# Optimization experiments

Hardware: AMD Instinct MI355X
Metric: run time of the kernel (lower is better)

The kernel has to match this reference:

```python
import jax, jax.numpy as jnp
import numpy as np

HIDDEN = 1024
K_STRIDE = 4


def setup_inputs() -> dict:
    key = jax.random.key(0)
    ks = jax.random.split(key, 12)
    N = 8192
    inp = {
        "speech_embed": jax.random.normal(ks[0], (N, HIDDEN * K_STRIDE), dtype=jnp.float32),
        "text_embed": jax.random.normal(ks[1], (N, HIDDEN), dtype=jnp.float32),
        # conv1d(1,1,kernel_size=1,bias=False) weight -> a single scalar
        "conv_w": jax.random.normal(ks[2], (), dtype=jnp.float32),
        # torch Linear weights stored as [in, out] for x @ W + b
        "Wq": jax.random.normal(ks[3], (HIDDEN, HIDDEN), dtype=jnp.float32) * (HIDDEN ** -0.5),
        "bq": jax.random.normal(ks[4], (HIDDEN,), dtype=jnp.float32) * 0.02,
        "Wk": jax.random.normal(ks[5], (HIDDEN, HIDDEN), dtype=jnp.float32) * (HIDDEN ** -0.5),
        "bk": jax.random.normal(ks[6], (HIDDEN,), dtype=jnp.float32) * 0.02,
        "Wv": jax.random.normal(ks[7], (HIDDEN, HIDDEN), dtype=jnp.float32) * (HIDDEN ** -0.5),
        "bv": jax.random.normal(ks[8], (HIDDEN,), dtype=jnp.float32) * 0.02,
        "Wo": jax.random.normal(ks[9], (HIDDEN, HIDDEN), dtype=jnp.float32) * (HIDDEN ** -0.5),
        "bo": jax.random.normal(ks[10], (HIDDEN,), dtype=jnp.float32) * 0.02,
    }
    return inp


def _attention(q, k, v, Wq, bq, Wk, bk, Wv, bv, Wo, bo):
    # Faithful to original: NO 1/sqrt(d) scaling, mask is None.
    q = q @ Wq + bq          # [N, H]
    k = k @ Wk + bk          # [N, H]
    v = v @ Wv + bv          # [N, H]
    weights = jax.nn.softmax(q @ k.T, axis=-1)  # [N, N]
    out = (weights @ v) @ Wo + bo               # [N, H]
    return out, weights


def reference(speech_embed, text_embed, conv_w, Wq, bq, Wk, bk, Wv, bv, Wo, bo):
    # conv1d kernel_size=1, stride=K, no bias == strided subsample * scalar weight
    speech = speech_embed[:, ::K_STRIDE] * conv_w  # [N, HIDDEN]
    tts_out, tts_w = _attention(text_embed, speech, speech,
                                Wq, bq, Wk, bk, Wv, bv, Wo, bo)
    stt_out, stt_w = _attention(speech, text_embed, text_embed,
                                Wq, bq, Wk, bk, Wv, bv, Wo, bo)
    return (tts_out, tts_w, stt_out, stt_w)
```

## Files before the change

### kernel.cpp

```cpp
#include <hip/hip_runtime.h>

#define HID 1024
#define NROW 8192
#define NCAT 16384

typedef unsigned short u16;
typedef short s16x8 __attribute__((ext_vector_type(8)));
typedef float f32x4 __attribute__((ext_vector_type(4)));

__device__ __forceinline__ u16 rtn16(float x) {
  unsigned xb = __builtin_bit_cast(unsigned, x);
  return (u16)((xb + 0x7fffu + ((xb >> 16) & 1u)) >> 16);
}
__device__ __forceinline__ float fromh(u16 h) {
  return __builtin_bit_cast(float, (unsigned)h << 16);
}
__device__ __forceinline__ void split2(float x, u16 &h, u16 &l) {
  h = rtn16(x);
  l = rtn16(x - fromh(h));
}

__device__ __forceinline__ void gl16(const void* g, void* l) {
  __builtin_amdgcn_global_load_lds(
      (const __attribute__((address_space(1))) unsigned int*)g,
      (__attribute__((address_space(3))) unsigned int*)l, 16, 0, 0);
}

template<int N> __device__ __forceinline__ void waitvm() {
  if constexpr (N == 3) asm volatile("s_waitcnt vmcnt(3)" ::: "memory");
  else if constexpr (N == 4) asm volatile("s_waitcnt vmcnt(4)" ::: "memory");
  else if constexpr (N == 5) asm volatile("s_waitcnt vmcnt(5)" ::: "memory");
  else if constexpr (N == 6) asm volatile("s_waitcnt vmcnt(6)" ::: "memory");
}

template<int ROWS>
__device__ __forceinline__ void stage_chunk(const u16* __restrict__ pg, int ld,
                                            int grow0, int k0, u16* ldsbase, int tid)
{
  constexpr int NLD = (ROWS * 32) / (512 * 8);
  #pragma unroll
  for (int j = 0; j < NLD; ++j) {
    int idx = tid + j * 512;
    int row = idx >> 2, q = idx & 3;
    int qs = q ^ ((row >> 1) & 3);
    gl16(pg + (size_t)(grow0 + row) * ld + k0 + qs * 8, ldsbase + (size_t)idx * 8);
  }
}

template<int NFR>
__device__ __forceinline__ void read_frags(s16x8* f, const u16* base,
                                           int w0, int fr, int fq)
{
  #pragma unroll
  for (int i = 0; i < NFR; ++i) {
    int r = w0 + i * 16 + fr;
    f[i] = *(const s16x8*)(base + r * 32 + ((fq ^ ((r >> 1) & 3)) << 3));
  }
}

template<int BN, int WMv, int WNv, int MF, int NF, bool OUT_SPLIT>
__global__ void __launch_bounds__(512, 2)
gemm_big(const u16* __restrict__ Agh, const u16* __restrict__ Agl, int lda,
         const u16* __restrict__ Bgh, const u16* __restrict__ Bgl, int ldb,
         float* __restrict__ Cf, u16* __restrict__ Ch, u16* __restrict__ Cl,
         int ldc, int K, int tiles_n)
{
  constexpr int BM = 256;
  constexpr int ASZ = BM * 32;
  constexpr int BSZ = BN * 32;
  constexpr int BUF = 2 * ASZ + 2 * BSZ;
  constexpr int AL_ = (ASZ * 2) / (512 * 16);
  constexpr int BL_ = (BSZ * 2) / (512 * 16);
  constexpr int TL  = 2 * AL_ + 2 * BL_;
  constexpr int W1 = TL - (AL_ + BL_);
  constexpr int W2 = TL - BL_;
  constexpr int W3 = AL_ + 2 * BL_;

  __shared__ __align__(16) u16 lds[2 * BUF];

  const int tid = threadIdx.x;
  const unsigned nwg = gridDim.x;
  const unsigned bid = blockIdx.x;
  const unsigned swz = (bid & 7u) * (nwg >> 3) + (bid >> 3);
  const int bm = (int)(swz / (unsigned)tiles_n) * BM;
  const int bn = (int)(swz % (unsigned)tiles_n) * BN;

  const int w = tid >> 6, lane = tid & 63;
  const int wr = (w / WNv) * (BM / WMv);
  const int wc = (w % WNv) * (BN / WNv);
  const int fr = lane & 15, fq = lane >> 4;

  f32x4 acc[MF][NF] = {};
  const int nt = K / 32;

  stage_chunk<BM>(Agh, lda, bm, 0, lds + 0,             tid);
  stage_chunk<BN>(Bgh, ldb, bn, 0, lds + 2 * ASZ,       tid);
  stage_chunk<BN>(Bgl, ldb, bn, 0, lds + 2 * ASZ + BSZ, tid);
  stage_chunk<BM>(Agl, lda, bm, 0, lds + ASZ,           tid);

  int cur = 0;
  for (int t = 0; t < nt; ++t) {
    const int k0n = (t + 1 == nt) ? 0 : (t + 1) * 32;
    const int nxt = cur ^ 1;
    u16* cb = lds + cur * BUF;
    u16* nb = lds + nxt * BUF;
    s16x8 ah[MF], bh[NF];

    waitvm<W1>();
    __builtin_amdgcn_s_barrier();
    __builtin_amdgcn_sched_barrier(0);
    stage_chunk<BM>(Agh, lda, bm, k0n, nb + 0,       tid);
    stage_chunk<BN>(Bgh, ldb, bn, k0n, nb + 2 * ASZ, tid);
    read_frags<MF>(ah, cb + 0,       wr, fr, fq);
    read_frags<NF>(bh, cb + 2 * ASZ, wc, fr, fq);
    __builtin_amdgcn_s_setprio(1);
    #pragma unroll
    for (int m = 0; m < MF; ++m)
      #pragma unroll
      for (int n = 0; n < NF; ++n)
        acc[m][n] = __builtin_amdgcn_mfma_f32_16x16x32_bf16(ah[m], bh[n], acc[m][n], 0, 0, 0);
    __builtin_amdgcn_s_setprio(0);

    waitvm<W2>();
    __builtin_amdgcn_s_barrier();
    __builtin_amdgcn_sched_barrier(0);
    stage_chunk<BN>(Bgl, ldb, bn, k0n, nb + 2 * ASZ + BSZ, tid);
    {
      s16x8 bl[NF];
      read_frags<NF>(bl, cb + 2 * ASZ + BSZ, wc, fr, fq);
      __builtin_amdgcn_s_setprio(1);
      #pragma unroll
      for (int m = 0; m < MF; ++m)
        #pragma unroll
        for (int n = 0; n < NF; ++n)
          acc[m][n] = __builtin_amdgcn_mfma_f32_16x16x32_bf16(ah[m], bl[n], acc[m][n], 0, 0, 0);
      __builtin_amdgcn_s_setprio(0);
    }

    waitvm<W3>();
    __builtin_amdgcn_s_barrier();
    __builtin_amdgcn_sched_barrier(0);
    stage_chunk<BM>(Agl, lda, bm, k0n, nb + ASZ, tid);
    {
      s16x8 al[MF];
      read_frags<MF>(al, cb + ASZ, wr, fr, fq);
      __builtin_amdgcn_s_setprio(1);
      #pragma unroll
      for (int m = 0; m < MF; ++m)
        #pragma unroll
        for (int n = 0; n < NF; ++n)
          acc[m][n] = __builtin_amdgcn_mfma_f32_16x16x32_bf16(al[m], bh[n], acc[m][n], 0, 0, 0);
      __builtin_amdgcn_s_setprio(0);
    }
    cur = nxt;
  }

  #pragma unroll
  for (int m = 0; m < MF; ++m) {
    int row0 = bm + wr + m * 16 + fq * 4;
    #pragma unroll
    for (int n = 0; n < NF; ++n) {
      int col = bn + wc + n * 16 + fr;
      if constexpr (OUT_SPLIT) {
        #pragma unroll
        for (int i = 0; i < 4; ++i) {
          u16 h, l; split2(acc[m][n][i], h, l);
          Ch[(size_t)(row0 + i) * ldc + col] = h;
          Cl[(size_t)(row0 + i) * ldc + col] = l;
        }
      } else {
        #pragma unroll
        for (int i = 0; i < 4; ++i)
          Cf[(size_t)(row0 + i) * ldc + col] = acc[m][n][i];
      }
    }
  }
}

template<int AMODE, bool ADD_BIAS, bool WRITE_T, bool OUT_SPLIT>
__global__ void __launch_bounds__(256, 2)
gemm_bt(const u16* __restrict__ Agh, const u16* __restrict__ Agl,
        const float* __restrict__ Agf, int lda,
        const u16* __restrict__ Bgh, const u16* __restrict__ Bgl, int ldb,
        const float* __restrict__ bias,
        float* __restrict__ Cf, u16* __restrict__ Ch, u16* __restrict__ Cl,
        int ldc, int K, int tiles_n)
{
  __shared__ __align__(16) u16 sAh[128 * 32];
  __shared__ __align__(16) u16 sAl[128 * 32];
  __shared__ __align__(16) u16 sBh[128 * 32];
  __shared__ __align__(16) u16 sBl[128 * 32];

  const int tid = threadIdx.x;
  const unsigned nwg = gridDim.x;
  const unsigned bid = blockIdx.x;
  const unsigned swz = (bid & 7u) * (nwg >> 3) + (bid >> 3);
  const int bm = (int)(swz / (unsigned)tiles_n) * 128;
  const int bn = (int)(swz % (unsigned)tiles_n) * 128;

  const int wave = tid >> 6;
  const int lane = tid & 63;
  const int wr = (wave >> 1) * 64;
  const int wc = (wave & 1) * 64;
  const int fr = lane & 15;
  const int fq = lane >> 4;

  const u16* pAh[2]; const u16* pAl[2];
  const u16* pBh[2]; const u16* pBl[2];
  u16* dA[2]; u16* dB[2];
  #pragma unroll
  for (int j = 0; j < 2; ++j) {
    int c = tid + j * 256;
    int row = c >> 2;
    int kc = (c & 3) * 8;
    if constexpr (AMODE == 0) {
      pAh[j] = Agh + (size_t)(bm + row) * lda + kc;
      pAl[j] = Agl + (size_t)(bm + row) * lda + kc;
    }
    pBh[j] = Bgh + (size_t)(bn + row) * ldb + kc;
    pBl[j] = Bgl + (size_t)(bn + row) * ldb + kc;
    dA[j] = (u16*)((char*)sAh + (size_t)c * 16);
    dB[j] = (u16*)((char*)sBh + (size_t)c * 16);
  }
  const size_t loOffA = (char*)sAl - (char*)sAh;
  const size_t loOffB = (char*)sBl - (char*)sBh;

  f32x4 acc[4][4] = {};

  for (int k0 = 0; k0 < K; k0 += 32) {
    if constexpr (AMODE == 0) {
      #pragma unroll
      for (int j = 0; j < 2; ++j) {
        gl16(pAh[j] + k0, dA[j]);
        gl16(pAl[j] + k0, (char*)dA[j] + loOffA);
        gl16(pBh[j] + k0, dB[j]);
        gl16(pBl[j] + k0, (char*)dB[j] + loOffB);
      }
    } else {
      #pragma unroll
      for (int j = 0; j < 2; ++j) {
        gl16(pBh[j] + k0, dB[j]);
        gl16(pBl[j] + k0, (char*)dB[j] + loOffB);
      }
      const int row = tid >> 1;
      const int c0 = (tid & 1) * 16;
      const float4* src = (const float4*)(Agf + (size_t)(bm + row) * lda + k0 + c0);
      u16* dh = &sAh[row * 32 + c0];
      u16* dl = &sAl[row * 32 + c0];
      #pragma unroll
      for (int q = 0; q < 4; ++q) {
        float4 v = src[q];
        ushort4 h4, l4;
        split2(v.x, h4.x, l4.x); split2(v.y, h4.y, l4.y);
        split2(v.z, h4.z, l4.z); split2(v.w, h4.w, l4.w);
        ((ushort4*)dh)[q] = h4;
        ((ushort4*)dl)[q] = l4;
      }
    }
    __syncthreads();

    s16x8 ah[4], al[4], bh[4], bl[4];
    #pragma unroll
    for (int m = 0; m < 4; ++m) {
      int r = (wr + m * 16 + fr) * 32 + fq * 8;
      ah[m] = *(const s16x8*)&sAh[r];
      al[m] = *(const s16x8*)&sAl[r];
    }
    #pragma unroll
    for (int n = 0; n < 4; ++n) {
      int r = (wc + n * 16 + fr) * 32 + fq * 8;
      bh[n] = *(const s16x8*)&sBh[r];
      bl[n] = *(const s16x8*)&sBl[r];
    }
    #pragma unroll
    for (int m = 0; m < 4; ++m)
      #pragma unroll
      for (int n = 0; n < 4; ++n) {
        acc[m][n] = __builtin_amdgcn_mfma_f32_16x16x32_bf16(ah[m], bh[n], acc[m][n], 0, 0, 0);
        acc[m][n] = __builtin_amdgcn_mfma_f32_16x16x32_bf16(ah[m], bl[n], acc[m][n], 0, 0, 0);
        acc[m][n] = __builtin_amdgcn_mfma_f32_16x16x32_bf16(al[m], bh[n], acc[m][n], 0, 0, 0);
      }
    __syncthreads();
  }

  #pragma unroll
  for (int m = 0; m < 4; ++m) {
    int row0 = bm + wr + m * 16 + fq * 4;
    #pragma unroll
    for (int n = 0; n < 4; ++n) {
      int col = bn + wc + n * 16 + fr;
      f32x4 v = acc[m][n];
      if (ADD_BIAS) v = v + bias[col];
      if constexpr (WRITE_T) {
        ushort4 h4, l4;
        split2(v[0], h4.x, l4.x); split2(v[1], h4.y, l4.y);
        split2(v[2], h4.z, l4.z); split2(v[3], h4.w, l4.w);
        *(ushort4*)&Ch[(size_t)col * ldc + row0] = h4;
        *(ushort4*)&Cl[(size_t)col * ldc + row0] = l4;
      } else if constexpr (OUT_SPLIT) {
        #pragma unroll
        for (int i = 0; i < 4; ++i) {
          u16 h, l; split2(v[i], h, l);
          Ch[(size_t)(row0 + i) * ldc + col] = h;
          Cl[(size_t)(row0 + i) * ldc + col] = l;
        }
      } else {
        #pragma unroll
        for (int i = 0; i < 4; ++i)
          Cf[(size_t)(row0 + i) * ldc + col] = v[i];
      }
    }
  }
}

template<bool SPLIT>
__global__ void __launch_bounds__(256)
softmax_rows(float* __restrict__ S, ushort4* __restrict__ Wh, ushort4* __restrict__ Wl)
{
  __shared__ float redm[4];
  __shared__ float reds[4];
  const int tid = threadIdx.x;
  float* p = S + (size_t)blockIdx.x * NROW;

  float4 v[8];
  float mx = -3.4e38f;
  #pragma unroll
  for (int i = 0; i < 8; ++i) {
    v[i] = *(const float4*)(p + ((tid + i * 256) << 2));
    mx = fmaxf(mx, fmaxf(fmaxf(v[i].x, v[i].y), fmaxf(v[i].z, v[i].w)));
  }
  #pragma unroll
  for (int off = 32; off > 0; off >>= 1)
    mx = fmaxf(mx, __shfl_xor(mx, off));
  if ((tid & 63) == 0) redm[tid >> 6] = mx;
  __syncthreads();
  mx = fmaxf(fmaxf(redm[0], redm[1]), fmaxf(redm[2], redm[3]));

  const float c = 1.44269504088896340736f;
  float s = 0.0f;
  #pragma unroll
  for (int i = 0; i < 8; ++i) {
    v[i].x = exp2f((v[i].x - mx) * c);
    v[i].y = exp2f((v[i].y - mx) * c);
    v[i].z = exp2f((v[i].z - mx) * c);
    v[i].w = exp2f((v[i].w - mx) * c);
    s += v[i].x + v[i].y + v[i].z + v[i].w;
  }
  #pragma unroll
  for (int off = 32; off > 0; off >>= 1)
    s += __shfl_xor(s, off);
  if ((tid & 63) == 0) reds[tid >> 6] = s;
  __syncthreads();
  s = reds[0] + reds[1] + reds[2] + reds[3];
  const float inv = 1.0f / s;
  const size_t rb4 = (size_t)blockIdx.x * (NROW / 4);

  #pragma unroll
  for (int i = 0; i < 8; ++i) {
    float4 w4;
    w4.x = v[i].x * inv; w4.y = v[i].y * inv;
    w4.z = v[i].z * inv; w4.w = v[i].w * inv;
    *(float4*)(p + ((tid + i * 256) << 2)) = w4;
    if constexpr (SPLIT) {
      ushort4 h4, l4;
      split2(w4.x, h4.x, l4.x); split2(w4.y, h4.y, l4.y);
      split2(w4.z, h4.z, l4.z); split2(w4.w, h4.w, l4.w);
      size_t o = rb4 + tid + i * 256;
      Wh[o] = h4;
      Wl[o] = l4;
    }
  }
}

__global__ void __launch_bounds__(256)
conv_split(const float4* __restrict__ in, const float* __restrict__ wp,
           ushort4* __restrict__ oh, ushort4* __restrict__ ol)
{
  const int i = blockIdx.x * 256 + threadIdx.x;
  const float w = wp[0];
  float a = in[i * 4 + 0].x * w, b = in[i * 4 + 1].x * w;
  float c = in[i * 4 + 2].x * w, d = in[i * 4 + 3].x * w;
  ushort4 h4, l4;
  split2(a, h4.x, l4.x); split2(b, h4.y, l4.y);
  split2(c, h4.z, l4.z); split2(d, h4.w, l4.w);
  oh[i] = h4;
  ol[i] = l4;
}

__global__ void __launch_bounds__(256)
split_mat(const float4* __restrict__ in, ushort4* __restrict__ oh, ushort4* __restrict__ ol)
{
  const int i = blockIdx.x * 256 + threadIdx.x;
  float4 v = in[i];
  ushort4 h4, l4;
  split2(v.x, h4.x, l4.x); split2(v.y, h4.y, l4.y);
  split2(v.z, h4.z, l4.z); split2(v.w, h4.w, l4.w);
  oh[i] = h4;
  ol[i] = l4;
}

__global__ void __launch_bounds__(256)
transpose_split(const float* __restrict__ in, u16* __restrict__ oh, u16* __restrict__ ol)
{
  __shared__ float t[32][33];
  const int tx = threadIdx.x & 31, ty = threadIdx.x >> 5;
  const int bx = blockIdx.x * 32, by = blockIdx.y * 32;
  #pragma unroll
  for (int i = 0; i < 32; i += 8)
    t[ty + i][tx] = in[(size_t)(by + ty + i) * HID + bx + tx];
  __syncthreads();
  #pragma unroll
  for (int i = 0; i < 32; i += 8) {
    float v = t[tx][ty + i];
    size_t o = (size_t)(bx + ty + i) * HID + by + tx;
    u16 h, l; split2(v, h, l);
    oh[o] = h;
    ol[o] = l;
  }
}

extern "C" void kernel_launch(void* const* d_in, const int* in_sizes, int n_in,
                              void* d_out, int out_size, void* d_ws, size_t ws_size,
                              hipStream_t stream)
{
  (void)in_sizes; (void)n_in; (void)out_size;
  const float* speech_embed = (const float*)d_in[0];
  const float* text  = (const float*)d_in[1];
  const float* convw = (const float*)d_in[2];
  const float* Wq = (const float*)d_in[3];
  const float* bq = (const float*)d_in[4];
  const float* Wk = (const float*)d_in[5];
  const float* bk = (const float*)d_in[6];
  const float* Wv = (const float*)d_in[7];
  const float* bv = (const float*)d_in[8];
  const float* Wo = (const float*)d_in[9];
  const float* bo = (const float*)d_in[10];
  float* out = (float*)d_out;

  const size_t NH = (size_t)NROW * HID;
  const size_t NN = (size_t)NROW * NROW;
  const size_t HH = (size_t)HID * HID;

  u16* base = (u16*)d_ws;
  size_t off = 0;
  auto alloc = [&](size_t n) { u16* p = base + off; off += n; return p; };
  u16 *cath = alloc(2 * NH), *catl = alloc(2 * NH);
  u16 *sph = cath,       *spl = catl;
  u16 *txh = cath + NH,  *txl = catl + NH;
  u16 *wqh = alloc(HH), *wql = alloc(HH);
  u16 *wkh = alloc(HH), *wkl = alloc(HH);
  u16 *wvh = alloc(HH), *wvl = alloc(HH);
  u16 *woh = alloc(HH), *wol = alloc(HH);
  u16 *qh = alloc(2 * NH), *ql = alloc(2 * NH);
  u16 *kh = alloc(2 * NH), *kl = alloc(2 * NH);
  u16 *vth = alloc(2 * NH), *vtl = alloc(2 * NH);
  u16 *c1h = qh,      *c1l = ql;
  u16 *c2h = qh + NH, *c2l = ql + NH;
  const bool pathA = ((off + 2 * NN) * sizeof(u16)) <= ws_size;
  u16 *wsh = nullptr, *wsl = nullptr;
  if (pathA) { wsh = alloc(NN); wsl = alloc(NN); }

  float* tts_out = out;
  float* tts_w   = out + NH;
  float* stt_out = tts_w + NN;
  float* stt_w   = stt_out + NH;

  const dim3 blk(256);
  const dim3 blk5(512);

  conv_split<<<NH / 1024, blk, 0, stream>>>((const float4*)speech_embed, convw,
                                            (ushort4*)sph, (ushort4*)spl);
  split_mat<<<NH / 1024, blk, 0, stream>>>((const float4*)text, (ushort4*)txh, (ushort4*)txl);
  const dim3 tg(32, 32);
  transpose_split<<<tg, blk, 0, stream>>>(Wq, wqh, wql);
  transpose_split<<<tg, blk, 0, stream>>>(Wk, wkh, wkl);
  transpose_split<<<tg, blk, 0, stream>>>(Wv, wvh, wvl);
  transpose_split<<<tg, blk, 0, stream>>>(Wo, woh, wol);

  const int gC = (NCAT / 128) * (HID / 128);
  const int gP = (NROW / 128) * (HID / 128);
  const int gS_big = (NROW / 256) * (NROW / 256);
  const int gPV_big = (NROW / 256) * (HID / 128);

  gemm_bt<0, true, false, true><<<gC, blk, 0, stream>>>(cath, catl, nullptr, HID, wqh, wql, HID, bq, nullptr, qh, ql, HID, HID, 8);
  gemm_bt<0, true, false, true><<<gC, blk, 0, stream>>>(cath, catl, nullptr, HID, wkh, wkl, HID, bk, nullptr, kh, kl, HID, HID, 8);
  gemm_bt<0, true, true,  true><<<gC, blk, 0, stream>>>(cath, catl, nullptr, HID, wvh, wvl, HID, bv, nullptr, vth, vtl, NCAT, HID, 8);

  gemm_big<256, 2, 4, 8, 4, false><<<gS_big, blk5, 0, stream>>>(
      qh + NH, ql + NH, HID, kh, kl, HID, tts_w, nullptr, nullptr, NROW, HID, 32);
  gemm_big<256, 2, 4, 8, 4, false><<<gS_big, blk5, 0, stream>>>(
      qh, ql, HID, kh + NH, kl + NH, HID, stt_w, nullptr, nullptr, NROW, HID, 32);

  if (pathA) {
    softmax_rows<true><<<NROW, blk, 0, stream>>>(tts_w, (ushort4*)wsh, (ushort4*)wsl);
    gemm_big<128, 4, 2, 4, 4, true><<<gPV_big, blk5, 0, stream>>>(
        wsh, wsl, NROW, vth, vtl, NCAT, nullptr, c1h, c1l, HID, NROW, 8);
    gemm_bt<0, true, false, false><<<gP, blk, 0, stream>>>(c1h, c1l, nullptr, HID, woh, wol, HID, bo, tts_out, nullptr, nullptr, HID, HID, 8);
    softmax_rows<true><<<NROW, blk, 0, stream>>>(stt_w, (ushort4*)wsh, (ushort4*)wsl);
    gemm_big<128, 4, 2, 4, 4, true><<<gPV_big, blk5, 0, stream>>>(
        wsh, wsl, NROW, vth + NROW, vtl + NROW, NCAT, nullptr, c2h, c2l, HID, NROW, 8);
    gemm_bt<0, true, false, false><<<gP, blk, 0, stream>>>(c2h, c2l, nullptr, HID, woh, wol, HID, bo, stt_out, nullptr, nullptr, HID, HID, 8);
  } else {
    softmax_rows<false><<<NROW, blk, 0, stream>>>(tts_w, nullptr, nullptr);
    softmax_rows<false><<<NROW, blk, 0, stream>>>(stt_w, nullptr, nullptr);
    gemm_bt<1, false, false, true><<<gP, blk, 0, stream>>>(nullptr, nullptr, tts_w, NROW, vth, vtl, NCAT, nullptr, nullptr, c1h, c1l, HID, NROW, 8);
    gemm_bt<0, true, false, false><<<gP, blk, 0, stream>>>(c1h, c1l, nullptr, HID, woh, wol, HID, bo, tts_out, nullptr, nullptr, HID, HID, 8);
    gemm_bt<1, false, false, true><<<gP, blk, 0, stream>>>(nullptr, nullptr, stt_w, NROW, vth + NROW, vtl + NROW, NCAT, nullptr, nullptr, c2h, c2l, HID, NROW, 8);
    gemm_bt<0, true, false, false><<<gP, blk, 0, stream>>>(c2h, c2l, nullptr, HID, woh, wol, HID, bo, stt_out, nullptr, nullptr, HID, HID, 8);
  }
}
```

Baseline: 2.804 ms.

## Drop split-bf16 precision for V, PV and output projections; use single bf16 plane

Switches the V projection, the softmax-weights times V product, and the output projection from three-MFMA split-bf16 emulation to plain bf16 with a single plane, and stops emitting low-plane copies of weights, V and softmax probabilities. Q/K projections move onto the larger 256-row tiled kernel with a bias epilogue, while QK^T keeps split precision because the unscaled logits feed a softmax. This cuts MFMA work, LDS traffic and memory writes for the value path, at the cost of reduced accuracy in the attention outputs.

Result: faster. 2.325 ms (-17.1%).

```diff
diff --git a/kernel.cpp b/kernel.cpp
--- a/kernel.cpp
+++ b/kernel.cpp
@@ -58,10 +58,11 @@
   }
 }
 
-template<int BN, int WMv, int WNv, int MF, int NF, bool OUT_SPLIT>
+template<int BN, int WMv, int WNv, int MF, int NF, bool ADD_BIAS, int OUTMODE>
 __global__ void __launch_bounds__(512, 2)
 gemm_big(const u16* __restrict__ Agh, const u16* __restrict__ Agl, int lda,
          const u16* __restrict__ Bgh, const u16* __restrict__ Bgl, int ldb,
+         const float* __restrict__ bias,
          float* __restrict__ Cf, u16* __restrict__ Ch, u16* __restrict__ Cl,
          int ldc, int K, int tiles_n)
 {
@@ -161,23 +162,25 @@
     #pragma unroll
     for (int n = 0; n < NF; ++n) {
       int col = bn + wc + n * 16 + fr;
-      if constexpr (OUT_SPLIT) {
+      f32x4 v = acc[m][n];
+      if (ADD_BIAS) v = v + bias[col];
+      if constexpr (OUTMODE == 1) {
         #pragma unroll
         for (int i = 0; i < 4; ++i) {
-          u16 h, l; split2(acc[m][n][i], h, l);
+          u16 h, l; split2(v[i], h, l);
           Ch[(size_t)(row0 + i) * ldc + col] = h;
           Cl[(size_t)(row0 + i) * ldc + col] = l;
         }
       } else {
         #pragma unroll
         for (int i = 0; i < 4; ++i)
-          Cf[(size_t)(row0 + i) * ldc + col] = acc[m][n][i];
+          Cf[(size_t)(row0 + i) * ldc + col] = v[i];
       }
     }
   }
 }
 
-template<int AMODE, bool ADD_BIAS, bool WRITE_T, bool OUT_SPLIT>
+template<int NPLANES, int AMODE, bool ADD_BIAS, int OUTMODE>
 __global__ void __launch_bounds__(256, 2)
 gemm_bt(const u16* __restrict__ Agh, const u16* __restrict__ Agl,
         const float* __restrict__ Agf, int lda,
@@ -186,10 +189,10 @@
         float* __restrict__ Cf, u16* __restrict__ Ch, u16* __restrict__ Cl,
         int ldc, int K, int tiles_n)
 {
-  __shared__ __align__(16) u16 sAh[128 * 32];
-  __shared__ __align__(16) u16 sAl[128 * 32];
-  __shared__ __align__(16) u16 sBh[128 * 32];
-  __shared__ __align__(16) u16 sBl[128 * 32];
+  constexpr int PL = 128 * 32;
+  __shared__ __align__(16) u16 lds[(NPLANES == 3 ? 4 : 2) * PL];
+  u16* const sAh = lds;
+  u16* const sBh = lds + (NPLANES == 3 ? 2 : 1) * PL;
 
   const int tid = threadIdx.x;
   const unsigned nwg = gridDim.x;
@@ -215,15 +218,13 @@
     int kc = (c & 3) * 8;
     if constexpr (AMODE == 0) {
       pAh[j] = Agh + (size_t)(bm + row) * lda + kc;
-      pAl[j] = Agl + (size_t)(bm + row) * lda + kc;
+      if constexpr (NPLANES == 3) pAl[j] = Agl + (size_t)(bm + row) * lda + kc;
     }
     pBh[j] = Bgh + (size_t)(bn + row) * ldb + kc;
-    pBl[j] = Bgl + (size_t)(bn + row) * ldb + kc;
-    dA[j] = (u16*)((char*)sAh + (size_t)c * 16);
-    dB[j] = (u16*)((char*)sBh + (size_t)c * 16);
-  }
-  const size_t loOffA = (char*)sAl - (char*)sAh;
-  const size_t loOffB = (char*)sBl - (char*)sBh;
+    if constexpr (NPLANES == 3) pBl[j] = Bgl + (size_t)(bn + row) * ldb + kc;
+    dA[j] = sAh + (size_t)c * 8;
+    dB[j] = sBh + (size_t)c * 8;
+  }
 
   f32x4 acc[4][4] = {};
 
@@ -232,54 +233,67 @@
       #pragma unroll
       for (int j = 0; j < 2; ++j) {
         gl16(pAh[j] + k0, dA[j]);
-        gl16(pAl[j] + k0, (char*)dA[j] + loOffA);
+        if constexpr (NPLANES == 3) gl16(pAl[j] + k0, dA[j] + PL);
         gl16(pBh[j] + k0, dB[j]);
-        gl16(pBl[j] + k0, (char*)dB[j] + loOffB);
+        if constexpr (NPLANES == 3) gl16(pBl[j] + k0, dB[j] + PL);
       }
     } else {
       #pragma unroll
       for (int j = 0; j < 2; ++j) {
         gl16(pBh[j] + k0, dB[j]);
-        gl16(pBl[j] + k0, (char*)dB[j] + loOffB);
+        if constexpr (NPLANES == 3) gl16(pBl[j] + k0, dB[j] + PL);
       }
       const int row = tid >> 1;
       const int c0 = (tid & 1) * 16;
       const float4* src = (const float4*)(Agf + (size_t)(bm + row) * lda + k0 + c0);
-      u16* dh = &sAh[row * 32 + c0];
-      u16* dl = &sAl[row * 32 + c0];
+      u16* dh = sAh + row * 32 + c0;
       #pragma unroll
       for (int q = 0; q < 4; ++q) {
         float4 v = src[q];
-        ushort4 h4, l4;
-        split2(v.x, h4.x, l4.x); split2(v.y, h4.y, l4.y);
-        split2(v.z, h4.z, l4.z); split2(v.w, h4.w, l4.w);
-        ((ushort4*)dh)[q] = h4;
-        ((ushort4*)dl)[q] = l4;
+        if constexpr (NPLANES == 3) {
+          ushort4 h4, l4;
+          split2(v.x, h4.x, l4.x); split2(v.y, h4.y, l4.y);
+          split2(v.z, h4.z, l4.z); split2(v.w, h4.w, l4.w);
+          ((ushort4*)dh)[q] = h4;
+          ((ushort4*)(dh + PL))[q] = l4;
+        } else {
+          ((ushort4*)dh)[q] = make_ushort4(rtn16(v.x), rtn16(v.y), rtn16(v.z), rtn16(v.w));
+        }
       }
     }
     __syncthreads();
 
-    s16x8 ah[4], al[4], bh[4], bl[4];
-    #pragma unroll
-    for (int m = 0; m < 4; ++m) {
-      int r = (wr + m * 16 + fr) * 32 + fq * 8;
-      ah[m] = *(const s16x8*)&sAh[r];
-      al[m] = *(const s16x8*)&sAl[r];
-    }
-    #pragma unroll
-    for (int n = 0; n < 4; ++n) {
-      int r = (wc + n * 16 + fr) * 32 + fq * 8;
-      bh[n] = *(const s16x8*)&sBh[r];
-      bl[n] = *(const s16x8*)&sBl[r];
-    }
+    s16x8 ah[4], bh[4];
     #pragma unroll
     for (int m = 0; m < 4; ++m)
-      #pragma unroll
-      for (int n = 0; n < 4; ++n) {
-        acc[m][n] = __builtin_amdgcn_mfma_f32_16x16x32_bf16(ah[m], bh[n], acc[m][n], 0, 0, 0);
-        acc[m][n] = __builtin_amdgcn_mfma_f32_16x16x32_bf16(ah[m], bl[n], acc[m][n], 0, 0, 0);
-        acc[m][n] = __builtin_amdgcn_mfma_f32_16x16x32_bf16(al[m], bh[n], acc[m][n], 0, 0, 0);
-      }
+      ah[m] = *(const s16x8*)(sAh + (wr + m * 16 + fr) * 32 + fq * 8);
+    #pragma unroll
+    for (int n = 0; n < 4; ++n)
+      bh[n] = *(const s16x8*)(sBh + (wc + n * 16 + fr) * 32 + fq * 8);
+
+    if constexpr (NPLANES == 3) {
+      s16x8 al[4], bl[4];
+      #pragma unroll
+      for (int m = 0; m < 4; ++m)
+        al[m] = *(const s16x8*)(sAh + PL + (wr + m * 16 + fr) * 32 + fq * 8);
+      #pragma unroll
+      for (int n = 0; n < 4; ++n)
+        bl[n] = *(const s16x8*)(sBh + PL + (wc + n * 16 + fr) * 32 + fq * 8);
+      #pragma unroll
+      for (int m = 0; m < 4; ++m)
+        #pragma unroll
+        for (int n = 0; n < 4; ++n) {
+          acc[m][n] = __builtin_amdgcn_mfma_f32_16x16x32_bf16(ah[m], bh[n], acc[m][n], 0, 0, 0);
+          acc[m][n] = __builtin_amdgcn_mfma_f32_16x16x32_bf16(ah[m], bl[n], acc[m][n], 0, 0, 0);
+          acc[m][n] = __builtin_amdgcn_mfma_f32_16x16x32_bf16(al[m], bh[n], acc[m][n], 0, 0, 0);
+        }
+    } else {
+      #pragma unroll
+      for (int m = 0; m < 4; ++m)
+        #pragma unroll
+        for (int n = 0; n < 4; ++n)
+          acc[m][n] = __builtin_amdgcn_mfma_f32_16x16x32_bf16(ah[m], bh[n], acc[m][n], 0, 0, 0);
+    }
     __syncthreads();
   }
 
@@ -291,31 +305,38 @@
       int col = bn + wc + n * 16 + fr;
       f32x4 v = acc[m][n];
       if (ADD_BIAS) v = v + bias[col];
-      if constexpr (WRITE_T) {
+      if constexpr (OUTMODE == 0) {
+        #pragma unroll
+        for (int i = 0; i < 4; ++i)
+          Cf[(size_t)(row0 + i) * ldc + col] = v[i];
+      } else if constexpr (OUTMODE == 1) {
+        #pragma unroll
+        for (int i = 0; i < 4; ++i) {
+          u16 h, l; split2(v[i], h, l);
+          Ch[(size_t)(row0 + i) * ldc + col] = h;
+          Cl[(size_t)(row0 + i) * ldc + col] = l;
+        }
+      } else if constexpr (OUTMODE == 2) {
         ushort4 h4, l4;
         split2(v[0], h4.x, l4.x); split2(v[1], h4.y, l4.y);
         split2(v[2], h4.z, l4.z); split2(v[3], h4.w, l4.w);
         *(ushort4*)&Ch[(size_t)col * ldc + row0] = h4;
         *(ushort4*)&Cl[(size_t)col * ldc + row0] = l4;
-      } else if constexpr (OUT_SPLIT) {
-        #pragma unroll
-        for (int i = 0; i < 4; ++i) {
-          u16 h, l; split2(v[i], h, l);
-          Ch[(size_t)(row0 + i) * ldc + col] = h;
-          Cl[(size_t)(row0 + i) * ldc + col] = l;
-        }
+      } else if constexpr (OUTMODE == 3) {
+        #pragma unroll
+        for (int i = 0; i < 4; ++i)
+          Ch[(size_t)(row0 + i) * ldc + col] = rtn16(v[i]);
       } else {
-        #pragma unroll
-        for (int i = 0; i < 4; ++i)
-          Cf[(size_t)(row0 + i) * ldc + col] = v[i];
+        *(ushort4*)&Ch[(size_t)col * ldc + row0] =
+            make_ushort4(rtn16(v[0]), rtn16(v[1]), rtn16(v[2]), rtn16(v[3]));
       }
     }
   }
 }
 
-template<bool SPLIT>
+template<bool EMITH>
 __global__ void __launch_bounds__(256)
-softmax_rows(float* __restrict__ S, ushort4* __restrict__ Wh, ushort4* __restrict__ Wl)
+softmax_rows(float* __restrict__ S, ushort4* __restrict__ Wh)
 {
   __shared__ float redm[4];
   __shared__ float reds[4];
@@ -361,14 +382,9 @@
     w4.x = v[i].x * inv; w4.y = v[i].y * inv;
     w4.z = v[i].z * inv; w4.w = v[i].w * inv;
     *(float4*)(p + ((tid + i * 256) << 2)) = w4;
-    if constexpr (SPLIT) {
-      ushort4 h4, l4;
-      split2(w4.x, h4.x, l4.x); split2(w4.y, h4.y, l4.y);
-      split2(w4.z, h4.z, l4.z); split2(w4.w, h4.w, l4.w);
-      size_t o = rb4 + tid + i * 256;
-      Wh[o] = h4;
-      Wl[o] = l4;
-    }
+    if constexpr (EMITH)
+      Wh[rb4 + tid + i * 256] =
+          make_ushort4(rtn16(w4.x), rtn16(w4.y), rtn16(w4.z), rtn16(w4.w));
   }
 }
 
@@ -399,6 +415,7 @@
   ol[i] = l4;
 }
 
+template<bool BOTH>
 __global__ void __launch_bounds__(256)
 transpose_split(const float* __restrict__ in, u16* __restrict__ oh, u16* __restrict__ ol)
 {
@@ -413,9 +430,12 @@
   for (int i = 0; i < 32; i += 8) {
     float v = t[tx][ty + i];
     size_t o = (size_t)(bx + ty + i) * HID + by + tx;
-    u16 h, l; split2(v, h, l);
-    oh[o] = h;
-    ol[o] = l;
+    if constexpr (BOTH) {
+      u16 h, l; split2(v, h, l);
+      oh[o] = h; ol[o] = l;
+    } else {
+      oh[o] = rtn16(v);
+    }
   }
 }
 
@@ -449,16 +469,16 @@
   u16 *txh = cath + NH,  *txl = catl + NH;
   u16 *wqh = alloc(HH), *wql = alloc(HH);
   u16 *wkh = alloc(HH), *wkl = alloc(HH);
-  u16 *wvh = alloc(HH), *wvl = alloc(HH);
-  u16 *woh = alloc(HH), *wol = alloc(HH);
+  u16 *wvh = alloc(HH);
+  u16 *woh = alloc(HH);
   u16 *qh = alloc(2 * NH), *ql = alloc(2 * NH);
   u16 *kh = alloc(2 * NH), *kl = alloc(2 * NH);
-  u16 *vth = alloc(2 * NH), *vtl = alloc(2 * NH);
-  u16 *c1h = qh,      *c1l = ql;
-  u16 *c2h = qh + NH, *c2l = ql + NH;
-  const bool pathA = ((off + 2 * NN) * sizeof(u16)) <= ws_size;
-  u16 *wsh = nullptr, *wsl = nullptr;
-  if (pathA) { wsh = alloc(NN); wsl = alloc(NN); }
+  u16 *vth = alloc(2 * NH);
+  u16 *c1h = qh;
+  u16 *c2h = qh + NH;
+  const bool pathA = ((off + NN) * sizeof(u16)) <= ws_size;
+  u16 *wsh = nullptr;
+  if (pathA) wsh = alloc(NN);
 
   float* tts_out = out;
   float* tts_w   = out + NH;
@@ -472,40 +492,69 @@
                                             (ushort4*)sph, (ushort4*)spl);
   split_mat<<<NH / 1024, blk, 0, stream>>>((const float4*)text, (ushort4*)txh, (ushort4*)txl);
   const dim3 tg(32, 32);
-  transpose_split<<<tg, blk, 0, stream>>>(Wq, wqh, wql);
-  transpose_split<<<tg, blk, 0, stream>>>(Wk, wkh, wkl);
-  transpose_split<<<tg, blk, 0, stream>>>(Wv, wvh, wvl);
-  transpose_split<<<tg, blk, 0, stream>>>(Wo, woh, wol);
-
-  const int gC = (NCAT / 128) * (HID / 128);
-  const int gP = (NROW / 128) * (HID / 128);
-  const int gS_big = (NROW / 256) * (NROW / 256);
-  const int gPV_big = (NROW / 256) * (HID / 128);
-
-  gemm_bt<0, true, false, true><<<gC, blk, 0, stream>>>(cath, catl, nullptr, HID, wqh, wql, HID, bq, nullptr, qh, ql, HID, HID, 8);
-  gemm_bt<0, true, false, true><<<gC, blk, 0, stream>>>(cath, catl, nullptr, HID, wkh, wkl, HID, bk, nullptr, kh, kl, HID, HID, 8);
-  gemm_bt<0, true, true,  true><<<gC, blk, 0, stream>>>(cath, catl, nullptr, HID, wvh, wvl, HID, bv, nullptr, vth, vtl, NCAT, HID, 8);
-
-  gemm_big<256, 2, 4, 8, 4, false><<<gS_big, blk5, 0, stream>>>(
-      qh + NH, ql + NH, HID, kh, kl, HID, tts_w, nullptr, nullptr, NROW, HID, 32);
-  gemm_big<256, 2, 4, 8, 4, false><<<gS_big, blk5, 0, stream>>>(
-      qh, ql, HID, kh + NH, kl + NH, HID, stt_w, nullptr, nullptr, NROW, HID, 32);
+  transpose_split<true ><<<tg, blk, 0, stream>>>(Wq, wqh, wql);
+  transpose_split<true ><<<tg, blk, 0, stream>>>(Wk, wkh, wkl);
+  transpose_split<false><<<tg, blk, 0, stream>>>(Wv, wvh, nullptr);
+  transpose_split<false><<<tg, blk, 0, stream>>>(Wo, woh, nullptr);
+
+  const int gProj = (NCAT / 256) * (HID / 128);
+  const int gVp   = (NCAT / 128) * (HID / 128);
+  const int gS    = (NROW / 256) * (NROW / 256);
+  const int gPV   = (NROW / 128) * (HID / 128);
 
   if (pathA) {
-    softmax_rows<true><<<NROW, blk, 0, stream>>>(tts_w, (ushort4*)wsh, (ushort4*)wsl);
-    gemm_big<128, 4, 2, 4, 4, true><<<gPV_big, blk5, 0, stream>>>(
-        wsh, wsl, NROW, vth, vtl, NCAT, nullptr, c1h, c1l, HID, NROW, 8);
-    gemm_bt<0, true, false, false><<<gP, blk, 0, stream>>>(c1h, c1l, nullptr, HID, woh, wol, HID, bo, tts_out, nullptr, nullptr, HID, HID, 8);
-    softmax_rows<true><<<NROW, blk, 0, stream>>>(stt_w, (ushort4*)wsh, (ushort4*)wsl);
-    gemm_big<128, 4, 2, 4, 4, true><<<gPV_big, blk5, 0, stream>>>(
-        wsh, wsl, NROW, vth + NROW, vtl + NROW, NCAT, nullptr, c2h, c2l, HID, NROW, 8);
-    gemm_bt<0, true, false, false><<<gP, blk, 0, stream>>>(c2h, c2l, nullptr, HID, woh, wol, HID, bo, stt_out, nullptr, nullptr, HID, HID, 8);
+    gemm_big<128, 4, 2, 4, 4, true, 1><<<gProj, blk5, 0, stream>>>(
+        cath, catl, HID, wqh, wql, HID, bq, nullptr, qh, ql, HID, HID, 8);
+    gemm_big<128, 4, 2, 4, 4, true, 1><<<gProj, blk5, 0, stream>>>(
+        cath, catl, HID, wkh, wkl, HID, bk, nullptr, kh, kl, HID, HID, 8);
+    gemm_bt<1, 0, true, 4><<<gVp, blk, 0, stream>>>(
+        cath, nullptr, nullptr, HID, wvh, nullptr, HID, bv,
+        nullptr, vth, nullptr, NCAT, HID, 8);
+
+    gemm_big<256, 2, 4, 8, 4, false, 0><<<gS, blk5, 0, stream>>>(
+        qh + NH, ql + NH, HID, kh, kl, HID, nullptr, tts_w, nullptr, nullptr, NROW, HID, 32);
+    gemm_big<256, 2, 4, 8, 4, false, 0><<<gS, blk5, 0, stream>>>(
+        qh, ql, HID, kh + NH, kl + NH, HID, nullptr, stt_w, nullptr, nullptr, NROW, HID, 32);
+
+    softmax_rows<true><<<NROW, blk, 0, stream>>>(tts_w, (ushort4*)wsh);
+    gemm_bt<1, 0, false, 3><<<gPV, blk, 0, stream>>>(
+        wsh, nullptr, nullptr, NROW, vth, nullptr, NCAT, nullptr,
+        nullptr, c1h, nullptr, HID, NROW, 8);
+    gemm_bt<1, 0, true, 0><<<gPV, blk, 0, stream>>>(
+        c1h, nullptr, nullptr, HID, woh, nullptr, HID, bo,
+        tts_out, nullptr, nullptr, HID, HID, 8);
+    softmax_rows<true><<<NROW, blk, 0, stream>>>(stt_w, (ushort4*)wsh);
+    gemm_bt<1, 0, false, 3><<<gPV, blk, 0, stream>>>(
+        wsh, nullptr, nullptr, NROW, vth + NROW, nullptr, NCAT, nullptr,
+        nullptr, c2h, nullptr, HID, NROW, 8);
+    gemm_bt<1, 0, true, 0><<<gPV, blk, 0, stream>>>(
+        c2h, nullptr, nullptr, HID, woh, nullptr, HID, bo,
+        stt_out, nullptr, nullptr, HID, HID, 8);
   } else {
-    softmax_rows<false><<<NROW, blk, 0, stream>>>(tts_w, nullptr, nullptr);
-    softmax_rows<false><<<NROW, blk, 0, stream>>>(stt_w, nullptr, nullptr);
-    gemm_bt<1, false, false, true><<<gP, blk, 0, stream>>>(nullptr, nullptr, tts_w, NROW, vth, vtl, NCAT, nullptr, nullptr, c1h, c1l, HID, NROW, 8);
-    gemm_bt<0, true, false, false><<<gP, blk, 0, stream>>>(c1h, c1l, nullptr, HID, woh, wol, HID, bo, tts_out, nullptr, nullptr, HID, HID, 8);
-    gemm_bt<1, false, false, true><<<gP, blk, 0, stream>>>(nullptr, nullptr, stt_w, NROW, vth + NROW, vtl + NROW, NCAT, nullptr, nullptr, c2h, c2l, HID, NROW, 8);
-    gemm_bt<0, true, false, false><<<gP, blk, 0, stream>>>(c2h, c2l, nullptr, HID, woh, wol, HID, bo, stt_out, nullptr, nullptr, HID, HID, 8);
-  }
-}
+    gemm_bt<3, 0, true, 1><<<gVp, blk, 0, stream>>>(
+        cath, catl, nullptr, HID, wqh, wql, HID, bq, nullptr, qh, ql, HID, HID, 8);
+    gemm_bt<3, 0, true, 1><<<gVp, blk, 0, stream>>>(
+        cath, catl, nullptr, HID, wkh, wkl, HID, bk, nullptr, kh, kl, HID, HID, 8);
+    gemm_bt<1, 0, true, 4><<<gVp, blk, 0, stream>>>(
+        cath, nullptr, nullptr, HID, wvh, nullptr, HID, bv,
+        nullptr, vth, nullptr, NCAT, HID, 8);
+    gemm_big<256, 2, 4, 8, 4, false, 0><<<gS, blk5, 0, stream>>>(
+        qh + NH, ql + NH, HID, kh, kl, HID, nullptr, tts_w, nullptr, nullptr, NROW, HID, 32);
+    gemm_big<256, 2, 4, 8, 4, false, 0><<<gS, blk5, 0, stream>>>(
+        qh, ql, HID, kh + NH, kl + NH, HID, nullptr, stt_w, nullptr, nullptr, NROW, HID, 32);
+    softmax_rows<false><<<NROW, blk, 0, stream>>>(tts_w, nullptr);
+    softmax_rows<false><<<NROW, blk, 0, stream>>>(stt_w, nullptr);
+    gemm_bt<1, 1, false, 3><<<gPV, blk, 0, stream>>>(
+        nullptr, nullptr, tts_w, NROW, vth, nullptr, NCAT, nullptr,
+        nullptr, c1h, nullptr, HID, NROW, 8);
+    gemm_bt<1, 0, true, 0><<<gPV, blk, 0, stream>>>(
+        c1h, nullptr, nullptr, HID, woh, nullptr, HID, bo,
+        tts_out, nullptr, nullptr, HID, HID, 8);
+    gemm_bt<1, 1, false, 3><<<gPV, blk, 0, stream>>>(
+        nullptr, nullptr, stt_w, NROW, vth + NROW, nullptr, NCAT, nullptr,
+        nullptr, c2h, nullptr, HID, NROW, 8);
+    gemm_bt<1, 0, true, 0><<<gPV, blk, 0, stream>>>(
+        c2h, nullptr, nullptr, HID, woh, nullptr, HID, bo,
+        stt_out, nullptr, nullptr, HID, HID, 8);
+  }
+}
```
